# Optimization experiments

Hardware: AMD Instinct MI355X
Metric: run time of the kernel (lower is better)

## Reference

```python
import jax, jax.numpy as jnp
import numpy as np

CH = 256
CQK = CH // 8
B, H, W = 4, 64, 64


def setup_inputs() -> dict:
    key = jax.random.key(0)
    ks = jax.random.split(key, 8)
    s_qk = 1.0 / np.sqrt(CH)  # MSR init for 1x1 conv: std = 1/sqrt(fan_in)
    x = jax.random.normal(ks[0], (B, CH, H, W), dtype=jnp.float32)
    Wq = jax.random.normal(ks[1], (CQK, CH), dtype=jnp.float32) * s_qk
    bq = jnp.zeros((CQK,), dtype=jnp.float32)
    Wk = jax.random.normal(ks[2], (CQK, CH), dtype=jnp.float32) * s_qk
    bk = jnp.zeros((CQK,), dtype=jnp.float32)
    Wv = jax.random.normal(ks[3], (CH, CH), dtype=jnp.float32) * s_qk
    bv = jnp.zeros((CH,), dtype=jnp.float32)
    # NOTE: module inits gamma=0; use a nonzero value so the attention branch is active
    gamma = jnp.float32(0.5) * jnp.ones((1,), dtype=jnp.float32)
    return {"x": x, "Wq": Wq, "bq": bq, "Wk": Wk, "bk": bk, "Wv": Wv, "bv": bv, "gamma": gamma}


def reference(x, Wq, bq, Wk, bk, Wv, bv, gamma):
    b, c, h, w = x.shape
    n = h * w
    xf = x.reshape(b, c, n)  # [B, C, N]
    # 1x1 convs are per-pixel channel projections
    q = jnp.einsum('oc,bcn->bon', Wq, xf) + bq[:, None]  # [B, C/8, N]
    k = jnp.einsum('oc,bcn->bon', Wk, xf) + bk[:, None]  # [B, C/8, N]
    v = jnp.einsum('oc,bcn->bon', Wv, xf) + bv[:, None]  # [B, C, N]
    # scores[b, i, j] = q[:, i] . k[:, j]  (no scaling, as in source)
    att = jax.nn.softmax(jnp.einsum('bci,bcj->bij', q, k), axis=-1)  # [B, N, N]
    out = jnp.einsum('bcj,bij->bci', v, att).reshape(b, c, h, w)
    return x + gamma[0] * out
```

## Files before the change

kernel.cpp:

```cpp
#include <hip/hip_runtime.h>
#include <hip/hip_bf16.h>

typedef unsigned short u16;
typedef __attribute__((ext_vector_type(8))) __bf16 bf16x8;
typedef __attribute__((ext_vector_type(8))) unsigned short u16x8;
typedef __attribute__((ext_vector_type(4))) float f32x4;
typedef __attribute__((ext_vector_type(16))) float f32x16;
typedef __attribute__((ext_vector_type(4))) unsigned int u32x4;
typedef __attribute__((ext_vector_type(2))) unsigned int u32x2;

#define MFMA16(a, b, c) __builtin_amdgcn_mfma_f32_16x16x32_bf16((a), (b), (c), 0, 0, 0)
#define MFMA32(a, b, c) __builtin_amdgcn_mfma_f32_32x32x16_bf16((a), (b), (c), 0, 0, 0)

#define BN 4
#define CH 256
#define CQK 32
#define NPIX 4096

__device__ __forceinline__ u16 f2bf(float f) {
    __hip_bfloat16 h = __float2bfloat16(f);
    return *reinterpret_cast<u16*>(&h);
}

__device__ __forceinline__ unsigned pack2(float a, float b) {
    return (unsigned)f2bf(a) | ((unsigned)f2bf(b) << 16);
}

__device__ __forceinline__ unsigned packtr(float a, float b) {
    return (__float_as_uint(b) & 0xffff0000u) | (__float_as_uint(a) >> 16);
}

__device__ __forceinline__ float bf2f(u16 v) {
    return __uint_as_float(((unsigned)v) << 16);
}

__device__ __forceinline__ f32x16 zero16() {
    f32x16 z;
#pragma unroll
    for (int i = 0; i < 16; ++i) z[i] = 0.f;
    return z;
}

__device__ __forceinline__ int perm16(int k) {
    return (k & 3) | ((k & 4) << 1) | ((k & 8) >> 1);
}

__global__ void k_transpose(const float* __restrict__ x, u16* __restrict__ xt) {
    __shared__ float xs[64][65];
    int n0 = blockIdx.x * 64, c0 = blockIdx.y * 64, b = blockIdx.z;
    int t = threadIdx.x;
    const float* xp = x + ((size_t)(b * CH + c0)) * NPIX + n0;
#pragma unroll
    for (int it = 0; it < 16; ++it) {
        int idx = it * 256 + t;
        int cc = idx >> 6, nn = idx & 63;
        xs[cc][nn] = xp[(size_t)cc * NPIX + nn];
    }
    __syncthreads();
    u16* op = xt + ((size_t)(b * NPIX + n0)) * CH + c0;
#pragma unroll
    for (int it = 0; it < 16; ++it) {
        int idx = it * 256 + t;
        int nn = idx >> 6, cc = idx & 63;
        op[(size_t)nn * CH + cc] = f2bf(xs[cc][nn]);
    }
}

__global__ void k_wcvt(const float* __restrict__ Wq, const float* __restrict__ Wk,
                       const float* __restrict__ Wv, u16* __restrict__ Wbf) {
    int idx = blockIdx.x * 256 + threadIdx.x;
    int o = idx >> 8, c = idx & 255;
    float v;
    if (o < 32) v = Wq[o * 256 + c];
    else if (o < 64) v = Wk[(o - 32) * 256 + c];
    else v = Wv[(o - 64) * 256 + c];
    Wbf[idx] = f2bf(v);
}

__launch_bounds__(256, 1)
__global__ void k_proj(const u16* __restrict__ Wbf, const u16* __restrict__ xt,
                       const float* __restrict__ bq, const float* __restrict__ bk,
                       const float* __restrict__ bv,
                       u16* __restrict__ qb, u16* __restrict__ kb, u16* __restrict__ vb) {
    int b = blockIdx.y, n0 = blockIdx.x * 64;
    int t = threadIdx.x, w = t >> 6, l = t & 63;
    int lr = l & 15, lg = l >> 4;

    f32x4 acc[5][4];
#pragma unroll
    for (int s = 0; s < 5; ++s)
#pragma unroll
        for (int u = 0; u < 4; ++u) acc[s][u] = f32x4{0.f, 0.f, 0.f, 0.f};

    const u16* xtb = xt + ((size_t)(b * NPIX + n0)) * CH;

#pragma unroll
    for (int kk = 0; kk < 8; ++kk) {
        int kof = kk * 32 + lg * 8;
        bf16x8 af[5], bfr[4];
#pragma unroll
        for (int s = 0; s < 5; ++s) {
            int o = w * 16 + s * 64 + lr;
            af[s] = *reinterpret_cast<const bf16x8*>(Wbf + (size_t)o * 256 + kof);
        }
#pragma unroll
        for (int u = 0; u < 4; ++u) {
            int n = u * 16 + lr;
            bfr[u] = *reinterpret_cast<const bf16x8*>(xtb + (size_t)n * CH + kof);
        }
#pragma unroll
        for (int s = 0; s < 5; ++s)
#pragma unroll
            for (int u = 0; u < 4; ++u) acc[s][u] = MFMA16(af[s], bfr[u], acc[s][u]);
    }

    int lrp = perm16(lr);
#pragma unroll
    for (int s = 0; s < 5; ++s) {
        int o0 = w * 16 + s * 64;
#pragma unroll
        for (int r = 0; r < 4; ++r) {
            int o = o0 + lg * 4 + r;
            float bias = (o < 32) ? bq[o] : (o < 64) ? bk[o - 32] : bv[o - 64];
#pragma unroll
            for (int u = 0; u < 4; ++u) {
                float val = acc[s][u][r] + bias;
                u16 h = f2bf(val);
                if (o < 32) qb[((size_t)b * NPIX + n0 + u * 16 + lr) * CQK + o] = h;
                else if (o < 64) kb[((size_t)b * NPIX + n0 + u * 16 + lr) * CQK + (o - 32)] = h;
                else {
                    int c = o - 64;
                    int jp = (u & 1) * 16 + lrp;
                    int s8 = jp >> 2, rem = jp & 3;
                    int jps = ((s8 ^ ((c >> 1) & 7)) << 2) | rem;
                    vb[((size_t)(b * CH + c)) * NPIX + n0 + (u >> 1) * 32 + jps] = h;
                }
            }
        }
    }
}

template <int NCHUNK>
__launch_bounds__(64, 2)
__global__ void k_attn7(const u16* __restrict__ qb, const u16* __restrict__ kb,
                        const u16* __restrict__ vb, const float* __restrict__ x,
                        const float* __restrict__ gamma,
                        u16* __restrict__ pacc, float* __restrict__ plsum,
                        float* __restrict__ out) {
    constexpr int JCH = NPIX / NCHUNK;
    constexpr int NT = JCH / 32;
    int xid = blockIdx.x;
    int it = xid >> 1, iq = xid & 1;
    int sc = blockIdx.y;
    int s = sc >> 1, ch = sc & 1;
    int b = blockIdx.z;
    int l = threadIdx.x;
    int lr = l & 31, hi = l >> 5;
    int i0 = it * 128 + iq * 64;
    int j0 = s * JCH;

    __shared__ u16 vlds[2][4096];
    __shared__ float lsl[64];

    bf16x8 qf[2][2];
#pragma unroll
    for (int is = 0; is < 2; ++is) {
        const u16* qrow = qb + ((size_t)b * NPIX + i0 + is * 32 + lr) * CQK;
        qf[is][0] = *(const bf16x8*)(qrow + hi * 8);
        qf[is][1] = *(const bf16x8*)(qrow + 16 + hi * 8);
    }

    const u16* kbase = kb + (size_t)b * NPIX * CQK;
    const u16* vsrc = vb + ((size_t)(b * CH + ch * 128 + (l >> 2))) * NPIX + j0 + (l & 3) * 8;

    f32x16 acc[2][4];
#pragma unroll
    for (int is = 0; is < 2; ++is)
#pragma unroll
        for (int ct = 0; ct < 4; ++ct) acc[is][ct] = zero16();
    float lsum[2] = {0.f, 0.f};

    bf16x8 kc0, kc1;
    auto kload = [&](int tt) {
        const u16* kr = kbase + (size_t)(j0 + tt * 32 + lr) * CQK;
        kc0 = *(const bf16x8*)(kr + hi * 8);
        kc1 = *(const bf16x8*)(kr + 16 + hi * 8);
    };
    auto dma = [&](int buf, int tt) {
#pragma unroll
        for (int m = 0; m < 8; ++m) {
            const u16* src = vsrc + (size_t)m * 16 * NPIX + tt * 32;
            __builtin_amdgcn_global_load_lds(
                (const __attribute__((address_space(1))) unsigned int*)src,
                (__attribute__((address_space(3))) unsigned int*)(&vlds[buf][m * 512]),
                16, 0, 0);
        }
    };
    auto qkexp = [&](bf16x8 (&pa)[4]) {
#pragma unroll
        for (int is = 0; is < 2; ++is) {
            f32x16 sf = MFMA32(kc0, qf[is][0], zero16());
            sf = MFMA32(kc1, qf[is][1], sf);
            float P[16];
#pragma unroll
            for (int e = 0; e < 16; ++e) {
                P[e] = __expf(sf[e] - 32.0f);
                lsum[is] += P[e];
            }
            u32x4 wa = {packtr(P[0], P[1]), packtr(P[2], P[3]),
                        packtr(P[4], P[5]), packtr(P[6], P[7])};
            u32x4 wc = {packtr(P[8], P[9]), packtr(P[10], P[11]),
                        packtr(P[12], P[13]), packtr(P[14], P[15])};
            pa[is * 2] = __builtin_bit_cast(bf16x8, wa);
            pa[is * 2 + 1] = __builtin_bit_cast(bf16x8, wc);
        }
    };
    auto pv = [&](int buf, bf16x8 (&pa)[4]) {
        const u16* base = &vlds[buf][0];
#pragma unroll
        for (int ct = 0; ct < 4; ++ct) {
            int row = ct * 32 + lr;
            int key = (row >> 1) & 7;
            const u32x2* rp = (const u32x2*)(base + row * 32);
            u32x2 e0 = rp[(2 * hi) ^ key];
            u32x2 e1 = rp[(2 * hi + 1) ^ key];
            u32x2 e2 = rp[(4 + 2 * hi) ^ key];
            u32x2 e3 = rp[(5 + 2 * hi) ^ key];
            u32x4 v0 = {e0[0], e0[1], e1[0], e1[1]};
            u32x4 v1 = {e2[0], e2[1], e3[0], e3[1]};
            bf16x8 vf0 = __builtin_bit_cast(bf16x8, v0);
            bf16x8 vf1 = __builtin_bit_cast(bf16x8, v1);
#pragma unroll
            for (int is = 0; is < 2; ++is) {
                acc[is][ct] = MFMA32(pa[is * 2], vf0, acc[is][ct]);
                acc[is][ct] = MFMA32(pa[is * 2 + 1], vf1, acc[is][ct]);
            }
        }
    };

    bf16x8 paA[4], paB[4];

    dma(0, 0);
    kload(0);
    qkexp(paA);
    kload(1);

    for (int tt = 0; tt < NT - 1; ++tt) {
        dma((tt + 1) & 1, tt + 1);
        qkexp(paB);
        kload(tt + 2 < NT ? tt + 2 : NT - 1);
        asm volatile("s_waitcnt vmcnt(10)" ::: "memory");
        __builtin_amdgcn_sched_barrier(0);
        pv(tt & 1, paA);
#pragma unroll
        for (int e = 0; e < 4; ++e) paA[e] = paB[e];
    }
    asm volatile("s_waitcnt vmcnt(0)" ::: "memory");
    __builtin_amdgcn_sched_barrier(0);
    pv((NT - 1) & 1, paA);

    lsum[0] += __shfl_xor(lsum[0], 32);
    lsum[1] += __shfl_xor(lsum[1], 32);

    if constexpr (NCHUNK == 1) {
        float g = gamma[0];
        if (l < 32) {
            lsl[l] = g / lsum[0];
            lsl[32 + l] = g / lsum[1];
        }
        asm volatile("s_waitcnt lgkmcnt(0)" ::: "memory");
#pragma unroll
        for (int is = 0; is < 2; ++is)
#pragma unroll
            for (int ct = 0; ct < 4; ++ct) {
                int c = ch * 128 + ct * 32 + lr;
                const float* xp = x + ((size_t)(b * CH + c)) * NPIX + i0;
                float* op = out + ((size_t)(b * CH + c)) * NPIX + i0;
#pragma unroll
                for (int r = 0; r < 16; ++r) {
                    int il = is * 32 + (r & 3) + 8 * (r >> 2) + 4 * hi;
                    op[il] = xp[il] + acc[is][ct][r] * lsl[il];
                }
            }
    } else {
        size_t pbase = ((((size_t)s * BN + b) * 32 + it) * 256) * 128;
#pragma unroll
        for (int is = 0; is < 2; ++is)
#pragma unroll
            for (int ct = 0; ct < 4; ++ct) {
                int c = ch * 128 + ct * 32 + lr;
#pragma unroll
                for (int q = 0; q < 4; ++q) {
                    int il0 = iq * 64 + is * 32 + 8 * q + 4 * hi;
                    u32x2 pr = {pack2(acc[is][ct][4 * q], acc[is][ct][4 * q + 1]),
                                pack2(acc[is][ct][4 * q + 2], acc[is][ct][4 * q + 3])};
                    *(u32x2*)(pacc + pbase + (size_t)c * 128 + il0) = pr;
                }
            }
        if (ch == 0 && l < 32) {
            size_t lb = (((size_t)s * BN + b) * 32 + it) * 128 + iq * 64;
            plsum[lb + l] = lsum[0];
            plsum[lb + 32 + l] = lsum[1];
        }
    }
}

template <int NCHUNK>
__global__ void k_reduce(const u16* __restrict__ pacc, const float* __restrict__ plsum,
                         const float* __restrict__ x, const float* __restrict__ gamma,
                         float* __restrict__ out) {
    int cg = blockIdx.x, it = blockIdx.y, b = blockIdx.z;
    int t = threadIdx.x;
    int c0 = cg * 32;
    __shared__ float invl[128];

    if (t < 128) {
        float lt = 0.f;
#pragma unroll
        for (int s = 0; s < NCHUNK; ++s)
            lt += plsum[(((size_t)s * BN + b) * 32 + it) * 128 + t];
        invl[t] = gamma[0] / lt;
    }
    __syncthreads();

    const size_t chunk_stride = (size_t)BN * 32 * 256 * 128;
    size_t base = (((size_t)b * 32 + it) * 256 + c0) * 128;

#pragma unroll
    for (int k = 0; k < 2; ++k) {
        int v = k * 256 + t;
        int cl = v >> 4;
        int io = (v & 15) * 8;
        size_t off = base + (size_t)cl * 128 + io;
        f32x4 a0 = {0.f, 0.f, 0.f, 0.f}, a1 = a0;
#pragma unroll
        for (int s = 0; s < NCHUNK; ++s) {
            u16x8 p = *(const u16x8*)(pacc + (size_t)s * chunk_stride + off);
            a0[0] += bf2f(p[0]); a0[1] += bf2f(p[1]); a0[2] += bf2f(p[2]); a0[3] += bf2f(p[3]);
            a1[0] += bf2f(p[4]); a1[1] += bf2f(p[5]); a1[2] += bf2f(p[6]); a1[3] += bf2f(p[7]);
        }
        f32x4 i0v = *(const f32x4*)(&invl[io]);
        f32x4 i1v = *(const f32x4*)(&invl[io + 4]);
        size_t oi = ((size_t)(b * CH + c0 + cl)) * NPIX + it * 128 + io;
        f32x4 x0 = *(const f32x4*)(x + oi);
        f32x4 x1 = *(const f32x4*)(x + oi + 4);
        *(f32x4*)(out + oi) = x0 + a0 * i0v;
        *(f32x4*)(out + oi + 4) = x1 + a1 * i1v;
    }
}

extern "C" void kernel_launch(void* const* d_in, const int* in_sizes, int n_in,
                              void* d_out, int out_size, void* d_ws, size_t ws_size,
                              hipStream_t stream) {
    const float* x = (const float*)d_in[0];
    const float* Wq = (const float*)d_in[1];
    const float* bq = (const float*)d_in[2];
    const float* Wk = (const float*)d_in[3];
    const float* bk = (const float*)d_in[4];
    const float* Wv = (const float*)d_in[5];
    const float* bv = (const float*)d_in[6];
    const float* gamma = (const float*)d_in[7];
    float* out = (float*)d_out;

    char* ws = (char*)d_ws;
    u16* xt = (u16*)(ws);
    u16* Wbf = (u16*)(ws + 8388608);
    u16* qb = (u16*)(ws + 8388608 + 163840);
    u16* kb = (u16*)(ws + 8388608 + 163840 + 1048576);
    u16* vb = (u16*)(ws + 8388608 + 163840 + 2097152);
    const size_t base_end = 8388608 + 163840 + 2097152 + 8388608;
    u16* pacc = (u16*)(ws + base_end);

    hipLaunchKernelGGL(k_transpose, dim3(64, 4, 4), dim3(256), 0, stream, x, xt);
    hipLaunchKernelGGL(k_wcvt, dim3(320), dim3(256), 0, stream, Wq, Wk, Wv, Wbf);
    hipLaunchKernelGGL(k_proj, dim3(64, 4), dim3(256), 0, stream, Wbf, xt, bq, bk, bv, qb, kb, vb);

    const size_t pacc4 = (size_t)4 * BN * NPIX * CH * 2;
    const size_t pls4 = (size_t)4 * BN * NPIX * 4;

    if (ws_size >= base_end + pacc4 + pls4) {
        float* plsum = (float*)(ws + base_end + pacc4);
        hipLaunchKernelGGL(k_attn7<4>, dim3(64, 8, 4), dim3(64), 0, stream,
                           qb, kb, vb, x, gamma, pacc, plsum, out);
        hipLaunchKernelGGL(k_reduce<4>, dim3(8, 32, 4), dim3(256), 0, stream,
                           pacc, plsum, x, gamma, out);
    } else {
        hipLaunchKernelGGL(k_attn7<1>, dim3(64, 2, 4), dim3(64), 0, stream,
                           qb, kb, vb, x, gamma, pacc, (float*)pacc, out);
    }
}
```

Before: 99.91 us.

## Share V tiles across two waves per block with triple-buffered LDS

The attention kernel now runs two waves per 128-thread block that cover adjacent 64-row query tiles. Each wave DMAs half of the shared V tile into LDS, so V is fetched from global memory once per block instead of once per wave, and the ring grows to three buffers with s_barrier synchronisation. The V swizzle moves from 8-byte to 16-byte granularity so the PV operands are read with single 128-bit LDS loads, and packtr uses v_perm. The cost is a barrier every tile and more LDS per block, which may reduce occupancy.

```diff
diff --git a/kernel.cpp b/kernel.cpp
--- a/kernel.cpp
+++ b/kernel.cpp
@@ -27,7 +27,7 @@
 }
 
 __device__ __forceinline__ unsigned packtr(float a, float b) {
-    return (__float_as_uint(b) & 0xffff0000u) | (__float_as_uint(a) >> 16);
+    return __builtin_amdgcn_perm(__float_as_uint(b), __float_as_uint(a), 0x07060302u);
 }
 
 __device__ __forceinline__ float bf2f(u16 v) {
@@ -131,8 +131,8 @@
                 else {
                     int c = o - 64;
                     int jp = (u & 1) * 16 + lrp;
-                    int s8 = jp >> 2, rem = jp & 3;
-                    int jps = ((s8 ^ ((c >> 1) & 7)) << 2) | rem;
+                    int sl = jp >> 3, off = jp & 7;
+                    int jps = ((sl ^ ((c >> 1) & 3)) << 3) | off;
                     vb[((size_t)(b * CH + c)) * NPIX + n0 + (u >> 1) * 32 + jps] = h;
                 }
             }
@@ -141,26 +141,25 @@
 }
 
 template <int NCHUNK>
-__launch_bounds__(64, 2)
-__global__ void k_attn7(const u16* __restrict__ qb, const u16* __restrict__ kb,
+__launch_bounds__(128, 2)
+__global__ void k_attn8(const u16* __restrict__ qb, const u16* __restrict__ kb,
                         const u16* __restrict__ vb, const float* __restrict__ x,
                         const float* __restrict__ gamma,
                         u16* __restrict__ pacc, float* __restrict__ plsum,
                         float* __restrict__ out) {
     constexpr int JCH = NPIX / NCHUNK;
     constexpr int NT = JCH / 32;
-    int xid = blockIdx.x;
-    int it = xid >> 1, iq = xid & 1;
+    int it = blockIdx.x;
     int sc = blockIdx.y;
     int s = sc >> 1, ch = sc & 1;
     int b = blockIdx.z;
-    int l = threadIdx.x;
+    int t = threadIdx.x, w = t >> 6, l = t & 63;
     int lr = l & 31, hi = l >> 5;
-    int i0 = it * 128 + iq * 64;
+    int i0 = it * 128 + w * 64;
     int j0 = s * JCH;
 
-    __shared__ u16 vlds[2][4096];
-    __shared__ float lsl[64];
+    __shared__ alignas(16) u16 vlds[3][4096];
+    __shared__ float lsl[2][64];
 
     bf16x8 qf[2][2];
 #pragma unroll
@@ -171,7 +170,8 @@
     }
 
     const u16* kbase = kb + (size_t)b * NPIX * CQK;
-    const u16* vsrc = vb + ((size_t)(b * CH + ch * 128 + (l >> 2))) * NPIX + j0 + (l & 3) * 8;
+    const u16* vsrc =
+        vb + ((size_t)(b * CH + ch * 128 + w * 64 + (l >> 2))) * NPIX + j0 + (l & 3) * 8;
 
     f32x16 acc[2][4];
 #pragma unroll
@@ -188,11 +188,12 @@
     };
     auto dma = [&](int buf, int tt) {
 #pragma unroll
-        for (int m = 0; m < 8; ++m) {
-            const u16* src = vsrc + (size_t)m * 16 * NPIX + tt * 32;
+        for (int mm = 0; mm < 4; ++mm) {
+            const u16* src = vsrc + (size_t)mm * 16 * NPIX + tt * 32;
             __builtin_amdgcn_global_load_lds(
                 (const __attribute__((address_space(1))) unsigned int*)src,
-                (__attribute__((address_space(3))) unsigned int*)(&vlds[buf][m * 512]),
+                (__attribute__((address_space(3))) unsigned int*)(
+                    &vlds[buf][(w * 64 + mm * 16) * 32]),
                 16, 0, 0);
         }
     };
@@ -220,16 +221,10 @@
 #pragma unroll
         for (int ct = 0; ct < 4; ++ct) {
             int row = ct * 32 + lr;
-            int key = (row >> 1) & 7;
-            const u32x2* rp = (const u32x2*)(base + row * 32);
-            u32x2 e0 = rp[(2 * hi) ^ key];
-            u32x2 e1 = rp[(2 * hi + 1) ^ key];
-            u32x2 e2 = rp[(4 + 2 * hi) ^ key];
-            u32x2 e3 = rp[(5 + 2 * hi) ^ key];
-            u32x4 v0 = {e0[0], e0[1], e1[0], e1[1]};
-            u32x4 v1 = {e2[0], e2[1], e3[0], e3[1]};
-            bf16x8 vf0 = __builtin_bit_cast(bf16x8, v0);
-            bf16x8 vf1 = __builtin_bit_cast(bf16x8, v1);
+            int key = (row >> 1) & 3;
+            const u16* rp = base + row * 32;
+            bf16x8 vf0 = *(const bf16x8*)(rp + ((hi ^ key) << 3));
+            bf16x8 vf1 = *(const bf16x8*)(rp + (((2 + hi) ^ key) << 3));
 #pragma unroll
             for (int is = 0; is < 2; ++is) {
                 acc[is][ct] = MFMA32(pa[is * 2], vf0, acc[is][ct]);
@@ -246,18 +241,20 @@
     kload(1);
 
     for (int tt = 0; tt < NT - 1; ++tt) {
-        dma((tt + 1) & 1, tt + 1);
+        dma((tt + 1) % 3, tt + 1);
         qkexp(paB);
         kload(tt + 2 < NT ? tt + 2 : NT - 1);
-        asm volatile("s_waitcnt vmcnt(10)" ::: "memory");
+        asm volatile("s_waitcnt vmcnt(6)" ::: "memory");
+        __builtin_amdgcn_s_barrier();
         __builtin_amdgcn_sched_barrier(0);
-        pv(tt & 1, paA);
+        pv(tt % 3, paA);
 #pragma unroll
         for (int e = 0; e < 4; ++e) paA[e] = paB[e];
     }
     asm volatile("s_waitcnt vmcnt(0)" ::: "memory");
+    __builtin_amdgcn_s_barrier();
     __builtin_amdgcn_sched_barrier(0);
-    pv((NT - 1) & 1, paA);
+    pv((NT - 1) % 3, paA);
 
     lsum[0] += __shfl_xor(lsum[0], 32);
     lsum[1] += __shfl_xor(lsum[1], 32);
@@ -265,9 +262,10 @@
     if constexpr (NCHUNK == 1) {
         float g = gamma[0];
         if (l < 32) {
-            lsl[l] = g / lsum[0];
-            lsl[32 + l] = g / lsum[1];
-        }
+            lsl[w][l] = g / lsum[0];
+        }
+        if (l >= 32) lsl[w][l] = 0.f;
+        if (l < 32) lsl[w][32 + l] = g / lsum[1];
         asm volatile("s_waitcnt lgkmcnt(0)" ::: "memory");
 #pragma unroll
         for (int is = 0; is < 2; ++is)
@@ -279,7 +277,7 @@
 #pragma unroll
                 for (int r = 0; r < 16; ++r) {
                     int il = is * 32 + (r & 3) + 8 * (r >> 2) + 4 * hi;
-                    op[il] = xp[il] + acc[is][ct][r] * lsl[il];
+                    op[il] = xp[il] + acc[is][ct][r] * lsl[w][il];
                 }
             }
     } else {
@@ -291,14 +289,14 @@
                 int c = ch * 128 + ct * 32 + lr;
 #pragma unroll
                 for (int q = 0; q < 4; ++q) {
-                    int il0 = iq * 64 + is * 32 + 8 * q + 4 * hi;
+                    int il0 = w * 64 + is * 32 + 8 * q + 4 * hi;
                     u32x2 pr = {pack2(acc[is][ct][4 * q], acc[is][ct][4 * q + 1]),
                                 pack2(acc[is][ct][4 * q + 2], acc[is][ct][4 * q + 3])};
                     *(u32x2*)(pacc + pbase + (size_t)c * 128 + il0) = pr;
                 }
             }
         if (ch == 0 && l < 32) {
-            size_t lb = (((size_t)s * BN + b) * 32 + it) * 128 + iq * 64;
+            size_t lb = (((size_t)s * BN + b) * 32 + it) * 128 + w * 64;
             plsum[lb + l] = lsum[0];
             plsum[lb + 32 + l] = lsum[1];
         }
@@ -380,12 +378,12 @@
 
     if (ws_size >= base_end + pacc4 + pls4) {
         float* plsum = (float*)(ws + base_end + pacc4);
-        hipLaunchKernelGGL(k_attn7<4>, dim3(64, 8, 4), dim3(64), 0, stream,
+        hipLaunchKernelGGL(k_attn8<4>, dim3(32, 8, 4), dim3(128), 0, stream,
                            qb, kb, vb, x, gamma, pacc, plsum, out);
         hipLaunchKernelGGL(k_reduce<4>, dim3(8, 32, 4), dim3(256), 0, stream,
                            pacc, plsum, x, gamma, out);
     } else {
-        hipLaunchKernelGGL(k_attn7<1>, dim3(64, 2, 4), dim3(64), 0, stream,
+        hipLaunchKernelGGL(k_attn8<1>, dim3(32, 2, 4), dim3(128), 0, stream,
                            qb, kb, vb, x, gamma, pacc, (float*)pacc, out);
     }
 }
```

Measured after the change: 94.57 us. 5.3% less time.
